# Kernel tuning notes

Hardware: AMD Instinct MI355X
Metric: run time of the kernel (lower is better)

The kernel has to match this reference:

```python
import jax, jax.numpy as jnp
import numpy as np


def extract_patches(x, k):
    # x: [B, C, H, W] -> patches [B, C, fh, fw, k, k]  (stride-1 VALID windows,
    # same layout as torch unfold(2,k,1).unfold(3,k,1))
    B, C, H, W = x.shape
    fh, fw = H - k + 1, W - k + 1
    rows = []
    for dy in range(k):  # k*k = 49 static slices, no data-dim python loop
        cols = [x[:, :, dy:dy + fh, dx:dx + fw] for dx in range(k)]
        rows.append(jnp.stack(cols, axis=-1))
    return jnp.stack(rows, axis=-2)  # [B, C, fh, fw, k, k]


def setup_inputs() -> dict:
    key = jax.random.key(0)
    k1, k2, k3 = jax.random.split(key, 3)
    B, Cin, H, W = 64, 3, 64, 64
    O, k = 16, 7
    stdv = 1.0 / float(np.sqrt(Cin * k * k))  # matches reset_parameters
    x = jax.random.normal(k1, (B, Cin, H, W), dtype=jnp.float32)
    K_hit = jax.random.uniform(k2, (O, Cin, k, k), jnp.float32, -stdv, stdv)
    K_miss = jax.random.uniform(k3, (O, Cin, k, k), jnp.float32, -stdv, stdv)
    return {"input": x, "K_hit": K_hit, "K_miss": K_miss}


def reference(input, K_hit, K_miss):
    B, Cin, H, W = input.shape
    O, _, k, _ = K_hit.shape
    fh = H - k + 1
    num_blocks = fh * fh * Cin  # as in the torch code (assumes square input)
    patches = extract_patches(input, k)  # [B, Cin, fh, fw, k, k]

    def body(carry, Ks):
        kh, km = Ks  # each [Cin, k, k]
        # F_hit = (patch - K_hit)*-1 ; (-relu(F_hit)).sum() == -sum(relu(K_hit - patch))
        s_hit = -jnp.sum(jax.nn.relu(kh[None, :, None, None, :, :] - patches))
        s_miss = jnp.sum(jax.nn.relu(patches - km[None, :, None, None, :, :]))
        return carry, (s_hit, s_miss)

    _, (s_hit, s_miss) = jax.lax.scan(body, None, (K_hit, K_miss))  # [O], [O]

    def tile(v):  # scalar per out channel broadcast over batch and all blocks
        t = jnp.broadcast_to(v[None, :, None], (B, O, num_blocks))
        return t.reshape(B, Cin * O, fh, fh)

    F_map = tile(s_hit - s_miss)
    F_hit_list = tile(s_hit)
    F_miss_list = tile(s_miss)
    return F_map, F_hit_list, F_miss_list
```

## Files before the change

### kernel.cpp

```cpp
#include <hip/hip_runtime.h>
#include <hip/hip_bf16.h>

#define NBUCK 2048
#define WB 0.005859375f
#define SCALE 170.6666667f

#define SEG 10092u
#define OSEG 161472u
#define OUT1 10334208u
#define NOUT 31002624u

#define TAIL_BASE (NOUT - 524288u)
#define P_TTAB 0u
#define P_STAB 245880u
#define P_PACK 246000u

typedef float v4f __attribute__((ext_vector_type(4)));

__global__ __launch_bounds__(1024) void build_kernel(
    const float* __restrict__ x, float* __restrict__ tail, float* __restrict__ gsum)
{
    __shared__ float sH[NBUCK];
    __shared__ float sWc[16], sWd[16];
    const int blk = blockIdx.x;
    const int c   = blk / 40;
    const int t40 = blk - c * 40;
    const int tid = threadIdx.x;
    sH[tid] = 0.f; sH[tid + 1024] = 0.f;
    if (blk == 0 && tid < 64) gsum[tid] = 0.f;
    __syncthreads();

    if (t40 < 16) {
        const int g = t40;
#pragma unroll
        for (int pb = 0; pb < 4; ++pb) {
            const int batch = g * 4 + pb;
            const int plane = batch * 3 + c;
            float4 val = ((const float4*)x)[plane * 1024 + tid];
            float vv[4] = {val.x, val.y, val.z, val.w};
            const int pix0 = tid * 4;
#pragma unroll
            for (int e = 0; e < 4; ++e) {
                const int idx = pix0 + e;
                const int py = idx >> 6, px = idx & 63;
                const float v = vv[e];
                const int b = min(max((int)fmaf(v, SCALE, 1024.f), 0), NBUCK - 1);
                atomicAdd(&sH[b], 1.f);
                const bool rb = (py < 6) | (py >= 58);
                const bool cb = (px < 6) | (px >= 58);
                if (rb & cb) {
                    const int ri = (py < 6) ? py : py - 52;
                    const int ci = (px < 6) ? px : px - 52;
                    tail[P_PACK + ((unsigned)c * 144 + ri * 12 + ci) * 64u + batch] = v;
                }
            }
        }
    } else if (t40 < 28) {
        const int ri = t40 - 16;
        const int py = (ri < 6) ? ri : ri + 52;
        const int b_ = tid >> 4, q = tid & 15;
        float4 val = ((const float4*)x)[(b_ * 3 + c) * 1024 + py * 16 + q];
        float vv[4] = {val.x, val.y, val.z, val.w};
#pragma unroll
        for (int e = 0; e < 4; ++e) {
            const int b = min(max((int)fmaf(vv[e], SCALE, 1024.f), 0), NBUCK - 1);
            atomicAdd(&sH[b], 1.f);
        }
    } else {
        const int ci = t40 - 28;
        const int px = (ci < 6) ? ci : ci + 52;
        const int b_ = tid >> 4, py0 = (tid & 15) * 4;
        const float* base = x + (b_ * 3 + c) * 4096 + px;
        float vr[4];
#pragma unroll
        for (int e = 0; e < 4; ++e) vr[e] = base[(py0 + e) * 64];
#pragma unroll
        for (int e = 0; e < 4; ++e) {
            const int b = min(max((int)fmaf(vr[e], SCALE, 1024.f), 0), NBUCK - 1);
            atomicAdd(&sH[b], 1.f);
        }
    }
    __syncthreads();

    const int lane = tid & 63;
    const int wid  = tid >> 6;
    const int b0 = 2 * tid, b1 = 2 * tid + 1;
    const float c0 = sH[b0], c1 = sH[b1];
    const float d0 = (float)b0 * c0, d1 = (float)b1 * c1;
    const float cs = c0 + c1, ds = d0 + d1;

    float ic = cs, id = ds;
#pragma unroll
    for (int off = 1; off < 64; off <<= 1) {
        const float tc = __shfl_up(ic, off);
        const float td = __shfl_up(id, off);
        if (lane >= off) { ic += tc; id += td; }
    }
    if (lane == 63) { sWc[wid] = ic; sWd[wid] = id; }
    __syncthreads();

    float baseC = 0.f, baseD = 0.f, Ntot = 0.f, Dtot = 0.f;
#pragma unroll
    for (int w = 0; w < 16; ++w) {
        const float wc = sWc[w], wd = sWd[w];
        Ntot += wc; Dtot += wd;
        if (w < wid) { baseC += wc; baseD += wd; }
    }
    const float Cex = baseC + ic - cs;
    const float Dex = baseD + id - ds;
    const float T0 = WB * (Dtot + 0.5f * Ntot);

    float* T = tail + P_TTAB + (unsigned)blk * 2049u;
    T[b0] = T0 + WB * (2.f * (float)b0 * Cex - 2.f * Dex - (float)b0 * Ntot);
    const float C1 = Cex + c0, D1 = Dex + d0;
    T[b1] = T0 + WB * (2.f * (float)b1 * C1 - 2.f * D1 - (float)b1 * Ntot);
    if (tid == 1023) {
        T[NBUCK] = T0 + WB * ((float)NBUCK * Ntot - 2.f * Dtot);
        tail[P_STAB + blk] = T0 - 6.f * Ntot;
    }
}

__global__ __launch_bounds__(256) void query_kernel(
    const float* __restrict__ Kh, const float* __restrict__ Km,
    const float* __restrict__ tail, float* __restrict__ gsum)
{
    __shared__ float sC[2304];
    __shared__ float sredA[32][8];
    __shared__ float sredL[32][8];

    const int c  = blockIdx.x / 49;
    const int t  = blockIdx.x - c * 49;
    const int dy = t / 7, dx = t - dy * 7;

#pragma unroll
    for (int ii = 0; ii < 9; ++ii) {
        const int i = ii * 256 + threadIdx.x;
        const int cell = i >> 6, batch = i & 63;
        const int qr = cell / 6, qc = cell - qr * 6;
        const int ri = (qr < dy) ? qr : 6 + qr;
        const int ci = (qc < dx) ? qc : 6 + qc;
        sC[i] = tail[P_PACK + ((unsigned)c * 144 + ri * 12 + ci) * 64u + batch];
    }
    __syncthreads();

    const int q  = threadIdx.x >> 3;
    const int sl = threadIdx.x & 7;
    const int hm = q >> 4, o = q & 15;
    const float k = (hm ? Km : Kh)[o * 147 + c * 49 + t];

    float accA = 0.f, accL = 0.f;
#pragma unroll 16
    for (int step = 0; step < 288; ++step) {
        const float v = sC[sl + 8 * step];
        accA += fabsf(k - v);
        accL += k - v;
    }

    {
        const float u = fmaf(k, SCALE, 1024.f);
        const int j = min(max((int)u, 0), NBUCK - 1);
        const float fr = u - (float)j;
        float A = 0.f, Sm = 0.f;
        for (int s = sl; s < 28; s += 8) {
            int slot; float sgn;
            if (s < 16)      { slot = s; sgn = 1.f; }
            else if (s < 22) { const int qq = s - 16; slot = 16 + ((qq < dy) ? qq : 6 + qq); sgn = -1.f; }
            else             { const int qq = s - 22; slot = 28 + ((qq < dx) ? qq : 6 + qq); sgn = -1.f; }
            const float* T = tail + P_TTAB + (unsigned)(c * 40 + slot) * 2049u;
            const float lerp = T[j] + fr * (T[j + 1] - T[j]);
            A  += sgn * lerp;
            Sm += sgn * tail[P_STAB + c * 40 + slot];
        }
        accA += A;
        accL -= Sm;
        if (sl == 0) accL += k * 212992.f;
    }
    sredA[q][sl] = accA;
    sredL[q][sl] = accL;
    __syncthreads();
    if (threadIdx.x < 64) {
        const int idx  = threadIdx.x >> 1;
        const int part = threadIdx.x & 1;
        const float (*sr)[8] = part ? sredL : sredA;
        float s = 0.f;
#pragma unroll
        for (int qq = 0; qq < 8; ++qq) s += sr[idx][qq];
        atomicAdd(&gsum[part * 32 + idx], s);
    }
}

__global__ __launch_bounds__(256) void fill_kernel(
    const float* __restrict__ gsum, v4f* __restrict__ out, unsigned n4)
{
    __shared__ float sv[48];
    if (threadIdx.x < 48) {
        const int o = threadIdx.x & 15, grp = threadIdx.x >> 4;
        const float h = -0.5f * (gsum[32 + o] + gsum[o]);
        const float m =  0.5f * (gsum[16 + o] - gsum[48 + o]);
        sv[threadIdx.x] = (grp == 0) ? (h - m) : ((grp == 1) ? h : m);
    }
    __syncthreads();
    const unsigned stride = gridDim.x * blockDim.x;
    for (unsigned i = blockIdx.x * blockDim.x + threadIdx.x; i < n4; i += stride) {
        const unsigned f = i * 4u;
        const unsigned w   = f / OUT1;
        const unsigned rem = f - w * OUT1;
        const unsigned o   = (rem % OSEG) / SEG;
        const float val = sv[w * 16 + o];
        v4f pk = {val, val, val, val};
        __builtin_nontemporal_store(pk, &out[i]);
    }
}

extern "C" void kernel_launch(void* const* d_in, const int* in_sizes, int n_in,
                              void* d_out, int out_size, void* d_ws, size_t ws_size,
                              hipStream_t stream)
{
    const float* x  = (const float*)d_in[0];
    const float* Kh = (const float*)d_in[1];
    const float* Km = (const float*)d_in[2];
    float* out  = (float*)d_out;
    float* tail = out + TAIL_BASE;
    float* gsum = (float*)d_ws;

    build_kernel<<<120, 1024, 0, stream>>>(x, tail, gsum);
    query_kernel<<<147, 256, 0, stream>>>(Kh, Km, tail, gsum);
    fill_kernel <<<4096, 256, 0, stream>>>(gsum, (v4f*)out, NOUT / 4u);
}
```

Measured before the change: 60.25 us.

## Transpose histogram tables and split build work across more blocks

The build kernel now uses 168 blocks, with each full-plane block handling 2 batches instead of 4. It writes the prefix tables in transposed, bucket-major layout split into full and row/column sections, so the query kernel can read neighboring slots with vectorized loads. The query kernel moves to 512 threads with 16 lanes per output pair, halving the per-thread loop over patch cells, and caches the kernel weights in shared memory. This adds strided, scattered stores in build in exchange for coalesced lookups and more parallelism in query.

```diff
diff --git a/kernel.cpp b/kernel.cpp
--- a/kernel.cpp
+++ b/kernel.cpp
@@ -11,9 +11,11 @@
 #define NOUT 31002624u
 
 #define TAIL_BASE (NOUT - 524288u)
-#define P_TTAB 0u
-#define P_STAB 245880u
-#define P_PACK 246000u
+#define F_TR   0u
+#define RC_TR  196704u
+#define SF_OFF 344232u
+#define SRC_OFF 344328u
+#define PACK   344400u
 
 typedef float v4f __attribute__((ext_vector_type(4)));
 
@@ -23,18 +25,19 @@
     __shared__ float sH[NBUCK];
     __shared__ float sWc[16], sWd[16];
     const int blk = blockIdx.x;
-    const int c   = blk / 40;
-    const int t40 = blk - c * 40;
     const int tid = threadIdx.x;
     sH[tid] = 0.f; sH[tid + 1024] = 0.f;
     if (blk == 0 && tid < 64) gsum[tid] = 0.f;
     __syncthreads();
 
-    if (t40 < 16) {
-        const int g = t40;
-#pragma unroll
-        for (int pb = 0; pb < 4; ++pb) {
-            const int batch = g * 4 + pb;
+    int slot, stride;
+    unsigned baseT, baseS;
+    if (blk < 96) {
+        const int c = blk / 32, g = blk % 32;
+        slot = c * 32 + g; stride = 96; baseT = F_TR; baseS = SF_OFF;
+#pragma unroll
+        for (int pb = 0; pb < 2; ++pb) {
+            const int batch = 2 * g + pb;
             const int plane = batch * 3 + c;
             float4 val = ((const float4*)x)[plane * 1024 + tid];
             float vv[4] = {val.x, val.y, val.z, val.w};
@@ -51,15 +54,17 @@
                 if (rb & cb) {
                     const int ri = (py < 6) ? py : py - 52;
                     const int ci = (px < 6) ? px : px - 52;
-                    tail[P_PACK + ((unsigned)c * 144 + ri * 12 + ci) * 64u + batch] = v;
+                    tail[PACK + ((unsigned)c * 144 + ri * 12 + ci) * 64u + batch] = v;
                 }
             }
         }
-    } else if (t40 < 28) {
-        const int ri = t40 - 16;
+    } else if (blk < 132) {
+        const int idx = blk - 96;
+        const int c = idx / 12, ri = idx % 12;
         const int py = (ri < 6) ? ri : ri + 52;
-        const int b_ = tid >> 4, q = tid & 15;
-        float4 val = ((const float4*)x)[(b_ * 3 + c) * 1024 + py * 16 + q];
+        slot = c * 24 + ri; stride = 72; baseT = RC_TR; baseS = SRC_OFF;
+        const int batch = tid >> 4, f4 = tid & 15;
+        float4 val = ((const float4*)x)[(batch * 3 + c) * 1024 + py * 16 + f4];
         float vv[4] = {val.x, val.y, val.z, val.w};
 #pragma unroll
         for (int e = 0; e < 4; ++e) {
@@ -67,10 +72,12 @@
             atomicAdd(&sH[b], 1.f);
         }
     } else {
-        const int ci = t40 - 28;
-        const int px = (ci < 6) ? ci : ci + 52;
-        const int b_ = tid >> 4, py0 = (tid & 15) * 4;
-        const float* base = x + (b_ * 3 + c) * 4096 + px;
+        const int idx = blk - 132;
+        const int c = idx / 12, ci = idx % 12;
+        const int pxc = (ci < 6) ? ci : ci + 52;
+        slot = c * 24 + 12 + ci; stride = 72; baseT = RC_TR; baseS = SRC_OFF;
+        const int batch = tid >> 4, py0 = (tid & 15) * 4;
+        const float* base = x + (batch * 3 + c) * 4096 + pxc;
         float vr[4];
 #pragma unroll
         for (int e = 0; e < 4; ++e) vr[e] = base[(py0 + e) * 64];
@@ -88,7 +95,6 @@
     const float c0 = sH[b0], c1 = sH[b1];
     const float d0 = (float)b0 * c0, d1 = (float)b1 * c1;
     const float cs = c0 + c1, ds = d0 + d1;
-
     float ic = cs, id = ds;
 #pragma unroll
     for (int off = 1; off < 64; off <<= 1) {
@@ -98,7 +104,6 @@
     }
     if (lane == 63) { sWc[wid] = ic; sWd[wid] = id; }
     __syncthreads();
-
     float baseC = 0.f, baseD = 0.f, Ntot = 0.f, Dtot = 0.f;
 #pragma unroll
     for (int w = 0; w < 16; ++w) {
@@ -110,81 +115,93 @@
     const float Dex = baseD + id - ds;
     const float T0 = WB * (Dtot + 0.5f * Ntot);
 
-    float* T = tail + P_TTAB + (unsigned)blk * 2049u;
-    T[b0] = T0 + WB * (2.f * (float)b0 * Cex - 2.f * Dex - (float)b0 * Ntot);
+    const float Tb0 = T0 + WB * (2.f * (float)b0 * Cex - 2.f * Dex - (float)b0 * Ntot);
     const float C1 = Cex + c0, D1 = Dex + d0;
-    T[b1] = T0 + WB * (2.f * (float)b1 * C1 - 2.f * D1 - (float)b1 * Ntot);
+    const float Tb1 = T0 + WB * (2.f * (float)b1 * C1 - 2.f * D1 - (float)b1 * Ntot);
+    tail[baseT + (unsigned)b0 * stride + slot] = Tb0;
+    tail[baseT + (unsigned)b1 * stride + slot] = Tb1;
     if (tid == 1023) {
-        T[NBUCK] = T0 + WB * ((float)NBUCK * Ntot - 2.f * Dtot);
-        tail[P_STAB + blk] = T0 - 6.f * Ntot;
-    }
-}
-
-__global__ __launch_bounds__(256) void query_kernel(
+        tail[baseT + (unsigned)NBUCK * stride + slot] =
+            T0 + WB * ((float)NBUCK * Ntot - 2.f * Dtot);
+        tail[baseS + slot] = T0 - 6.f * Ntot;
+    }
+}
+
+__global__ __launch_bounds__(512) void query_kernel(
     const float* __restrict__ Kh, const float* __restrict__ Km,
     const float* __restrict__ tail, float* __restrict__ gsum)
 {
     __shared__ float sC[2304];
-    __shared__ float sredA[32][8];
-    __shared__ float sredL[32][8];
+    __shared__ float sK[32];
+    __shared__ float sredA[32][16];
+    __shared__ float sredL[32][16];
 
     const int c  = blockIdx.x / 49;
     const int t  = blockIdx.x - c * 49;
     const int dy = t / 7, dx = t - dy * 7;
-
-#pragma unroll
-    for (int ii = 0; ii < 9; ++ii) {
-        const int i = ii * 256 + threadIdx.x;
+    const int tid = threadIdx.x;
+
+    for (int i = tid; i < 2304; i += 512) {
         const int cell = i >> 6, batch = i & 63;
         const int qr = cell / 6, qc = cell - qr * 6;
         const int ri = (qr < dy) ? qr : 6 + qr;
         const int ci = (qc < dx) ? qc : 6 + qc;
-        sC[i] = tail[P_PACK + ((unsigned)c * 144 + ri * 12 + ci) * 64u + batch];
-    }
-    __syncthreads();
-
-    const int q  = threadIdx.x >> 3;
-    const int sl = threadIdx.x & 7;
-    const int hm = q >> 4, o = q & 15;
-    const float k = (hm ? Km : Kh)[o * 147 + c * 49 + t];
+        sC[i] = tail[PACK + ((unsigned)c * 144 + ri * 12 + ci) * 64u + batch];
+    }
+    if (tid < 32)
+        sK[tid] = ((tid >= 16) ? Km : Kh)[(tid & 15) * 147 + c * 49 + t];
+    __syncthreads();
+
+    const int q   = tid >> 4;
+    const int sub = tid & 15;
+    const float k = sK[q];
 
     float accA = 0.f, accL = 0.f;
 #pragma unroll 16
-    for (int step = 0; step < 288; ++step) {
-        const float v = sC[sl + 8 * step];
+    for (int step = 0; step < 144; ++step) {
+        const float v = sC[sub + 16 * step];
         accA += fabsf(k - v);
         accL += k - v;
     }
 
-    {
-        const float u = fmaf(k, SCALE, 1024.f);
-        const int j = min(max((int)u, 0), NBUCK - 1);
-        const float fr = u - (float)j;
-        float A = 0.f, Sm = 0.f;
-        for (int s = sl; s < 28; s += 8) {
-            int slot; float sgn;
-            if (s < 16)      { slot = s; sgn = 1.f; }
-            else if (s < 22) { const int qq = s - 16; slot = 16 + ((qq < dy) ? qq : 6 + qq); sgn = -1.f; }
-            else             { const int qq = s - 22; slot = 28 + ((qq < dx) ? qq : 6 + qq); sgn = -1.f; }
-            const float* T = tail + P_TTAB + (unsigned)(c * 40 + slot) * 2049u;
-            const float lerp = T[j] + fr * (T[j + 1] - T[j]);
-            A  += sgn * lerp;
-            Sm += sgn * tail[P_STAB + c * 40 + slot];
-        }
-        accA += A;
-        accL -= Sm;
-        if (sl == 0) accL += k * 212992.f;
-    }
-    sredA[q][sl] = accA;
-    sredL[q][sl] = accL;
-    __syncthreads();
-    if (threadIdx.x < 64) {
-        const int idx  = threadIdx.x >> 1;
-        const int part = threadIdx.x & 1;
-        const float (*sr)[8] = part ? sredL : sredA;
+    const float u = fmaf(k, SCALE, 1024.f);
+    const int j = min(max((int)u, 0), NBUCK - 1);
+    const float fr = u - (float)j;
+
+    if (sub < 8) {
+        const v4f r0 = *(const v4f*)(tail + F_TR + (unsigned)j * 96u + c * 32 + sub * 4);
+        const v4f r1 = *(const v4f*)(tail + F_TR + (unsigned)(j + 1) * 96u + c * 32 + sub * 4);
+        const float s0 = r0.x + r0.y + r0.z + r0.w;
+        const float s1 = r1.x + r1.y + r1.z + r1.w;
+        accA += s0 + fr * (s1 - s0);
+        const v4f sf = *(const v4f*)(tail + SF_OFF + c * 32 + sub * 4);
+        accL -= sf.x + sf.y + sf.z + sf.w;
+        if (sub == 0) accL += k * 212992.f;
+    } else if (sub < 14) {
+        const int s6 = sub - 8;
+        const int rinv = (s6 < dy) ? s6 : 6 + s6;
+        const int cinv = (s6 < dx) ? s6 : 6 + s6;
+        const int slr = c * 24 + rinv;
+        const int slc = c * 24 + 12 + cinv;
+        const float tr0 = tail[RC_TR + (unsigned)j * 72u + slr];
+        const float tr1 = tail[RC_TR + (unsigned)(j + 1) * 72u + slr];
+        const float tc0 = tail[RC_TR + (unsigned)j * 72u + slc];
+        const float tc1 = tail[RC_TR + (unsigned)(j + 1) * 72u + slc];
+        accA -= tr0 + fr * (tr1 - tr0);
+        accA -= tc0 + fr * (tc1 - tc0);
+        accL += tail[SRC_OFF + slr] + tail[SRC_OFF + slc];
+    }
+
+    sredA[q][sub] = accA;
+    sredL[q][sub] = accL;
+    __syncthreads();
+    if (tid < 64) {
+        const int idx  = tid >> 1;
+        const int part = tid & 1;
+        const float (*sr)[16] = part ? sredL : sredA;
         float s = 0.f;
 #pragma unroll
-        for (int qq = 0; qq < 8; ++qq) s += sr[idx][qq];
+        for (int e = 0; e < 16; ++e) s += sr[idx][e];
         atomicAdd(&gsum[part * 32 + idx], s);
     }
 }
@@ -223,7 +240,7 @@
     float* tail = out + TAIL_BASE;
     float* gsum = (float*)d_ws;
 
-    build_kernel<<<120, 1024, 0, stream>>>(x, tail, gsum);
-    query_kernel<<<147, 256, 0, stream>>>(Kh, Km, tail, gsum);
+    build_kernel<<<168, 1024, 0, stream>>>(x, tail, gsum);
+    query_kernel<<<147, 512, 0, stream>>>(Kh, Km, tail, gsum);
     fill_kernel <<<4096, 256, 0, stream>>>(gsum, (v4f*)out, NOUT / 4u);
 }
```

Measured after the change: 53.84 us. 10.6% less time.
